# Kernel optimization log

Hardware: AMD Instinct MI355X
Metric: run time of the kernel (lower is better)

The kernel has to match this reference:

```python
import jax, jax.numpy as jnp
import numpy as np

N, D = 4096, 512
TAU, ALPHA, EPS = 0.2, 0.5, 1e-15
L2_EPS = 1e-12  # F.normalize eps


def setup_inputs() -> dict:
    key = jax.random.key(0)
    ks = jax.random.split(key, 12)
    # xavier_normal_ with gain=1.414 for [D, D] linears
    std = 1.414 * (2.0 / (D + D)) ** 0.5
    xn = lambda k: jax.random.normal(k, (D, D), jnp.float32) * std
    return {
        "z1": jax.random.normal(ks[0], (N, D), jnp.float32),
        "z2": jax.random.normal(ks[1], (N, D), jnp.float32),
        # local projector: Linear -> PReLU -> Linear
        "lw1": xn(ks[2]), "lb1": jnp.zeros((D,), jnp.float32),
        "la": jnp.full((1,), 0.25, jnp.float32),  # PReLU weight (torch default 0.25)
        "lw2": xn(ks[3]), "lb2": jnp.zeros((D,), jnp.float32),
        # global projector
        "gw1": xn(ks[4]), "gb1": jnp.zeros((D,), jnp.float32),
        "ga": jnp.full((1,), 0.25, jnp.float32),
        "gw2": xn(ks[5]), "gb2": jnp.zeros((D,), jnp.float32),
        # discriminator bilinear weight
        "W": xn(ks[6]),
        # binary positive-pair mask [N, N]
        "mask": jax.random.randint(ks[7], (N, N), 0, 2, jnp.int32),
    }


def _prelu(x, a):
    return jnp.where(x >= 0, x, a * x)


def _proj(z, w1, b1, a, w2, b2):
    # nn.Sequential(Linear, PReLU, Linear); torch Linear: z @ W.T + b
    return _prelu(z @ w1.T + b1, a[0]) @ w2.T + b2


def _l2norm(z):
    n = jnp.linalg.norm(z, axis=-1, keepdims=True)
    return z / jnp.maximum(n, L2_EPS)


def _infonce(h1, h2, m, tau):
    a = _l2norm(h1)
    b = _l2norm(h2)
    sim_intra = jnp.exp(a @ a.T / tau)  # [N, N]
    sim_inter = jnp.exp(a @ b.T / tau)  # [N, N]
    num = (sim_inter * m).sum(1)
    den = sim_intra.sum(1) + sim_inter.sum(1) - (sim_intra * m).sum(1)
    return (-jnp.log(num / den)).mean()


def reference(z1, z2, lw1, lb1, la, lw2, lb2, gw1, gb1, ga, gw2, gb2, W, mask):
    m = mask.astype(jnp.float32)
    # local (node-level) InfoNCE through the local projector
    h1 = _proj(z1, lw1, lb1, la, lw2, lb2)
    h2 = _proj(z2, lw1, lb1, la, lw2, lb2)
    local = 0.5 * (_infonce(h1, h2, m, TAU) + _infonce(h2, h1, m.T, TAU))

    # global (DGI-style) loss
    def gloss(pos_z, neg_z):
        s = pos_z.mean(0)                               # readout [D]
        h = _proj(s, gw1, gb1, ga, gw2, gb2)            # global projector [D]
        summ = W @ h                                    # [D]
        d_pos = jax.nn.sigmoid(pos_z @ summ)            # [N]
        d_neg = jax.nn.sigmoid(neg_z @ summ)            # [N]
        pos_loss = -jnp.log(d_pos + EPS).mean()
        neg_loss = -jnp.log(1.0 - d_neg + EPS).mean()
        return 0.5 * (pos_loss + neg_loss)

    glob = 0.5 * (gloss(z1, z2) + gloss(z2, z1))
    return ALPHA * local + (1.0 - ALPHA) * glob
```

## Files before the change

kernel.cpp:

```cpp
#include <hip/hip_runtime.h>
#include <math.h>

#define NN 4096
#define DD 512
#define INV_TAU 5.0f
#define EPSV 1e-15f

typedef unsigned short u16;
typedef __attribute__((ext_vector_type(8))) short short8;
typedef __attribute__((ext_vector_type(4))) float f32x4;

__device__ __forceinline__ void gld16(const void* g, void* l) {
  __builtin_amdgcn_global_load_lds(
      (const __attribute__((address_space(1))) unsigned int*)g,
      (__attribute__((address_space(3))) unsigned int*)l, 16, 0, 0);
}

__device__ __forceinline__ void bar_vm4() {
  asm volatile("s_waitcnt vmcnt(4) lgkmcnt(0)\n\ts_barrier" ::: "memory");
}
__device__ __forceinline__ void bar_vm2() {
  asm volatile("s_waitcnt vmcnt(2) lgkmcnt(0)\n\ts_barrier" ::: "memory");
}
__device__ __forceinline__ void bar_vm1() {
  asm volatile("s_waitcnt vmcnt(1) lgkmcnt(0)\n\ts_barrier" ::: "memory");
}
__device__ __forceinline__ void bar_vm0() {
  asm volatile("s_waitcnt vmcnt(0) lgkmcnt(0)\n\ts_barrier" ::: "memory");
}

__device__ __forceinline__ float bf2f(u16 u) {
  return __uint_as_float(((unsigned)u) << 16);
}
__device__ __forceinline__ u16 f2bf(float x) {
  unsigned u = __float_as_uint(x);
  u += 0x7fff + ((u >> 16) & 1);
  return (u16)(u >> 16);
}

__device__ __forceinline__ float wave_sum(float v) {
#pragma unroll
  for (int o = 32; o > 0; o >>= 1) v += __shfl_down(v, o, 64);
  return v;
}

__global__ __launch_bounds__(256) void tobf16cm(
    const float* __restrict__ a, const float* __restrict__ b,
    const float* __restrict__ c, const float* __restrict__ d2,
    u16* __restrict__ o, float* __restrict__ pc1, float* __restrict__ pc2,
    float* __restrict__ zbf) {
  const int bid = blockIdx.x, tid = threadIdx.x;
  if (bid >= 4608) {
    const int blk = bid - 4608;
    const int r0 = blk * 32;
    float a0 = 0.f, a1 = 0.f, c0 = 0.f, c1 = 0.f;
    for (int r = r0; r < r0 + 32; ++r) {
      const size_t ro = (size_t)r * DD;
      a0 += c[ro + tid];
      a1 += c[ro + 256 + tid];
      c0 += d2[ro + tid];
      c1 += d2[ro + 256 + tid];
    }
    pc1[blk * 512 + tid] = a0;
    pc1[blk * 512 + 256 + tid] = a1;
    pc2[blk * 512 + tid] = c0;
    pc2[blk * 512 + 256 + tid] = c1;
    return;
  }
  if (bid < 128) zbf[bid * 256 + tid] = 0.f;
  const int i = bid * 256 + tid;
  int j = i;
  const float* s;
  if (j < 65536) {
    s = a + (size_t)j * 4;
  } else {
    j -= 65536;
    if (j < 65536) {
      s = b + (size_t)j * 4;
    } else {
      j -= 65536;
      if (j < 524288) {
        s = c + (size_t)j * 4;
      } else {
        j -= 524288;
        s = d2 + (size_t)j * 4;
      }
    }
  }
  float4 v = *(const float4*)s;
  unsigned long long pk = (unsigned long long)f2bf(v.x) |
                          ((unsigned long long)f2bf(v.y) << 16) |
                          ((unsigned long long)f2bf(v.z) << 32) |
                          ((unsigned long long)f2bf(v.w) << 48);
  *(unsigned long long*)&o[(size_t)i * 4] = pk;
}

template <int ACT>
__global__ __launch_bounds__(512) void gemm_mfma(
    const u16* __restrict__ A, const u16* __restrict__ Bw,
    const float* __restrict__ bias, const float* __restrict__ alpha_p,
    u16* __restrict__ out) {
  __shared__ __align__(16) u16 sh[3 * 6144];
  const int tid = threadIdx.x, w = tid >> 6, lane = tid & 63;
  const int quad = lane >> 4, m16 = lane & 15;
  const int wi = w >> 1, wj = w & 1;
  const int bid = blockIdx.x;
  const int xcd = bid & 7, idx = bid >> 3;
  const int i0 = (4 * xcd + (idx & 3)) * 128;
  const int j0 = ((idx >> 2) & 7) * 64;
  const int bz = idx >> 5;
  const u16* Ab = A + (size_t)bz * ((size_t)NN * DD);
  u16* ob = out + (size_t)bz * ((size_t)NN * DD);
  const int roff =
      (m16 >> 1) * 64 + (((((m16 & 1) << 2) | quad) ^ (m16 >> 1)) * 8);
  const int st = (lane & 7) ^ (lane >> 3);
  const int srow = 2 * (lane >> 3) + (st >> 2);
  const int scol = (st & 3) * 8;
  const u16* gs = (w < 4) ? Ab : Bw;
  const int grow0 = ((w < 4) ? i0 + 2 * w * 16 : j0 + (w - 4) * 16) + srow;
  const int doff0 = (w < 4) ? 2 * w * 512 : 4096 + (w - 4) * 512;
  auto stage = [&](int bo, int k) {
    const int kn = k * 32;
    gld16(&gs[(size_t)grow0 * DD + kn + scol], sh + bo + doff0);
    if (w < 4)
      gld16(&gs[(size_t)(grow0 + 16) * DD + kn + scol], sh + bo + doff0 + 512);
  };
  stage(0, 0);
  stage(6144, 1);
  if (w < 4) bar_vm2(); else bar_vm1();
  f32x4 acc[2][2] = {};
  int ro = 0;
  for (int kc = 0; kc < 16; ++kc) {
    if (kc <= 13) {
      int so = ro + 12288;
      if (so >= 18432) so -= 18432;
      stage(so, kc + 2);
    }
    const u16* As = sh + ro;
    const u16* Bs = sh + ro + 4096;
    short8 ar[2], br[2];
#pragma unroll
    for (int s = 0; s < 2; ++s) {
      ar[s] = *(const short8*)&As[(wi * 32 + s * 16) * 32 + roff];
      br[s] = *(const short8*)&Bs[(wj * 32 + s * 16) * 32 + roff];
    }
    __builtin_amdgcn_s_setprio(1);
#pragma unroll
    for (int si = 0; si < 2; ++si)
#pragma unroll
      for (int sj = 0; sj < 2; ++sj)
        acc[si][sj] = __builtin_amdgcn_mfma_f32_16x16x32_bf16(
            ar[si], br[sj], acc[si][sj], 0, 0, 0);
    __builtin_amdgcn_s_setprio(0);
    if (kc <= 13) {
      if (w < 4) bar_vm2(); else bar_vm1();
    } else if (kc == 14) {
      bar_vm0();
    }
    ro += 6144;
    if (ro == 18432) ro = 0;
  }
  const float al = ACT ? alpha_p[0] : 0.f;
#pragma unroll
  for (int si = 0; si < 2; ++si)
#pragma unroll
    for (int sj = 0; sj < 2; ++sj) {
      const int col = j0 + wj * 32 + sj * 16 + m16;
      const float bv = bias[col];
#pragma unroll
      for (int r = 0; r < 4; ++r) {
        const int row = i0 + wi * 32 + si * 16 + quad * 4 + r;
        float x = acc[si][sj][r] + bv;
        if (ACT) x = (x >= 0.f) ? x : al * x;
        ob[(size_t)row * DD + col] = f2bf(x);
      }
    }
}

__global__ __launch_bounds__(256) void rownorm_bf16(const u16* __restrict__ h,
                                                    u16* __restrict__ o) {
  const int tid = threadIdx.x;
  const int row = blockIdx.x * 4 + (tid >> 6);
  const int lane = tid & 63;
  const size_t base = (size_t)row * DD + lane * 8;
  short8 v = *(const short8*)&h[base];
  float f[8];
  float s = 0.f;
#pragma unroll
  for (int j = 0; j < 8; ++j) {
    f[j] = bf2f((u16)v[j]);
    s += f[j] * f[j];
  }
  s = wave_sum(s);
  const float inv = 1.f / fmaxf(sqrtf(__shfl(s, 0, 64)), 1e-12f);
  short8 r;
#pragma unroll
  for (int j = 0; j < 8; ++j) r[j] = (short)f2bf(f[j] * inv);
  *(short8*)&o[base] = r;
}

__global__ __launch_bounds__(1024) void mv_chain(
    const float* __restrict__ pc1, const float* __restrict__ pc2,
    const float* __restrict__ gw1, const float* __restrict__ gb1,
    const float* __restrict__ ga, const float* __restrict__ gw2,
    const float* __restrict__ gb2, const float* __restrict__ W,
    float* __restrict__ summ1, float* __restrict__ summ2) {
  const int bz = blockIdx.x;
  const float* pc = bz ? pc2 : pc1;
  float* summ = bz ? summ2 : summ1;
  __shared__ float sv[512], tv[512], hv[512];
  const int tid = threadIdx.x;
  if (tid < 512) {
    float a = 0.f;
    for (int b = 0; b < 128; ++b) a += pc[b * 512 + tid];
    sv[tid] = a * (1.f / NN);
  }
  __syncthreads();
  const int w = tid >> 6, lane = tid & 63;
  for (int rq = 0; rq < 8; ++rq) {
    const int row = w * 32 + rq * 4;
    float a0 = 0.f, a1 = 0.f, a2 = 0.f, a3 = 0.f;
#pragma unroll
    for (int t = 0; t < 8; ++t) {
      const float x = sv[lane + 64 * t];
      a0 = fmaf(gw1[(size_t)(row + 0) * DD + lane + 64 * t], x, a0);
      a1 = fmaf(gw1[(size_t)(row + 1) * DD + lane + 64 * t], x, a1);
      a2 = fmaf(gw1[(size_t)(row + 2) * DD + lane + 64 * t], x, a2);
      a3 = fmaf(gw1[(size_t)(row + 3) * DD + lane + 64 * t], x, a3);
    }
    a0 = wave_sum(a0); a1 = wave_sum(a1); a2 = wave_sum(a2); a3 = wave_sum(a3);
    if (lane == 0) {
      const float al = ga[0];
      float v0 = a0 + gb1[row + 0], v1 = a1 + gb1[row + 1];
      float v2 = a2 + gb1[row + 2], v3 = a3 + gb1[row + 3];
      tv[row + 0] = (v0 >= 0.f) ? v0 : al * v0;
      tv[row + 1] = (v1 >= 0.f) ? v1 : al * v1;
      tv[row + 2] = (v2 >= 0.f) ? v2 : al * v2;
      tv[row + 3] = (v3 >= 0.f) ? v3 : al * v3;
    }
  }
  __syncthreads();
  for (int rq = 0; rq < 8; ++rq) {
    const int row = w * 32 + rq * 4;
    float a0 = 0.f, a1 = 0.f, a2 = 0.f, a3 = 0.f;
#pragma unroll
    for (int t = 0; t < 8; ++t) {
      const float x = tv[lane + 64 * t];
      a0 = fmaf(gw2[(size_t)(row + 0) * DD + lane + 64 * t], x, a0);
      a1 = fmaf(gw2[(size_t)(row + 1) * DD + lane + 64 * t], x, a1);
      a2 = fmaf(gw2[(size_t)(row + 2) * DD + lane + 64 * t], x, a2);
      a3 = fmaf(gw2[(size_t)(row + 3) * DD + lane + 64 * t], x, a3);
    }
    a0 = wave_sum(a0); a1 = wave_sum(a1); a2 = wave_sum(a2); a3 = wave_sum(a3);
    if (lane == 0) {
      hv[row + 0] = a0 + gb2[row + 0];
      hv[row + 1] = a1 + gb2[row + 1];
      hv[row + 2] = a2 + gb2[row + 2];
      hv[row + 3] = a3 + gb2[row + 3];
    }
  }
  __syncthreads();
  for (int rq = 0; rq < 8; ++rq) {
    const int row = w * 32 + rq * 4;
    float a0 = 0.f, a1 = 0.f, a2 = 0.f, a3 = 0.f;
#pragma unroll
    for (int t = 0; t < 8; ++t) {
      const float x = hv[lane + 64 * t];
      a0 = fmaf(W[(size_t)(row + 0) * DD + lane + 64 * t], x, a0);
      a1 = fmaf(W[(size_t)(row + 1) * DD + lane + 64 * t], x, a1);
      a2 = fmaf(W[(size_t)(row + 2) * DD + lane + 64 * t], x, a2);
      a3 = fmaf(W[(size_t)(row + 3) * DD + lane + 64 * t], x, a3);
    }
    a0 = wave_sum(a0); a1 = wave_sum(a1); a2 = wave_sum(a2); a3 = wave_sum(a3);
    if (lane == 0) {
      summ[row + 0] = a0;
      summ[row + 1] = a1;
      summ[row + 2] = a2;
      summ[row + 3] = a3;
    }
  }
}

__global__ __launch_bounds__(256) void logsigp(
    const float* __restrict__ z1, const float* __restrict__ z2,
    const float* __restrict__ sm1, const float* __restrict__ sm2,
    float* __restrict__ plsP, float* __restrict__ plsN) {
  const int ch = blockIdx.y;
  const float* z = ch ? z2 : z1;
  const float* sp = ch ? sm2 : sm1;
  const float* sn = ch ? sm1 : sm2;
  const int lane = threadIdx.x & 63;
  const int wid = threadIdx.x >> 6;
  const int row = blockIdx.x * 4 + wid;
  float dp = 0.f, dn = 0.f;
#pragma unroll
  for (int t = 0; t < 8; ++t) {
    const float zv = z[(size_t)row * DD + lane + 64 * t];
    dp = fmaf(zv, sp[lane + 64 * t], dp);
    dn = fmaf(zv, sn[lane + 64 * t], dn);
  }
  dp = wave_sum(dp);
  dn = wave_sum(dn);
  __shared__ float bp[4], bn[4];
  if (lane == 0) {
    const float sg = 1.f / (1.f + __expf(-dp));
    bp[wid] = -logf(sg + EPSV);
    const float sg2 = 1.f / (1.f + __expf(-dn));
    bn[wid] = -logf(1.f - sg2 + EPSV);
  }
  __syncthreads();
  if (threadIdx.x == 0) {
    plsP[ch * 1024 + blockIdx.x] = bp[0] + bp[1] + bp[2] + bp[3];
    plsN[ch * 1024 + blockIdx.x] = bn[0] + bn[1] + bn[2] + bn[3];
  }
}

__global__ __launch_bounds__(512) void sim_mfma(
    const u16* __restrict__ na, const u16* __restrict__ nb,
    const int* __restrict__ mask, float* __restrict__ zb) {
  extern __shared__ __align__(16) u16 shm[];
  const int tid = threadIdx.x;
  const int w = tid >> 6, lane = tid & 63;
  const int quad = lane >> 4, m16 = lane & 15;
  const int ig = w & 3, jh = w >> 2;
  const int i0 = blockIdx.y * 128, j0 = blockIdx.x * 128;
  const int roff =
      (m16 >> 1) * 64 + (((((m16 & 1) << 2) | quad) ^ (m16 >> 1)) * 8);
  const int st = (lane & 7) ^ (lane >> 3);
  const int srow = 2 * (lane >> 3) + (st >> 2);
  const int scol = (st & 3) * 8;
  const int p = w >> 1, rh = (w & 1) * 64;
  const u16* gs = (p & 1) ? nb : na;
  const int gr = ((p < 2) ? i0 : j0) + rh + srow;
  u16* dst0 = shm + p * 4096 + rh * 32;
  auto stage = [&](int bo, int k) {
    const int kn = k * 32;
#pragma unroll
    for (int rr = 0; rr < 64; rr += 16)
      gld16(&gs[(size_t)(gr + rr) * DD + kn + scol], dst0 + bo + rr * 32);
  };
  stage(0, 0);
  stage(16384, 1);
  bar_vm4();
  f32x4 a11[2][4] = {}, a12[2][4] = {}, a22[2][4] = {};
  int ro = 0;
  for (int kc = 0; kc < 16; ++kc) {
    if (kc <= 13) {
      int so = ro + 32768;
      if (so >= 49152) so -= 49152;
      stage(so, kc + 2);
    }
    const u16* Ai = shm + ro;
    const u16* Bi = shm + ro + 4096;
    const u16* Aj = shm + ro + 8192;
    const u16* Bj = shm + ro + 12288;
    short8 ai0 = *(const short8*)&Ai[(ig * 32) * 32 + roff];
    short8 ai1 = *(const short8*)&Ai[(ig * 32 + 16) * 32 + roff];
    short8 bi0 = *(const short8*)&Bi[(ig * 32) * 32 + roff];
    short8 bi1 = *(const short8*)&Bi[(ig * 32 + 16) * 32 + roff];
#pragma unroll
    for (int c = 0; c < 4; ++c) {
      short8 aj = *(const short8*)&Aj[(jh * 64 + c * 16) * 32 + roff];
      short8 bj = *(const short8*)&Bj[(jh * 64 + c * 16) * 32 + roff];
      __builtin_amdgcn_s_setprio(1);
      a11[0][c] = __builtin_amdgcn_mfma_f32_16x16x32_bf16(ai0, aj, a11[0][c], 0, 0, 0);
      a11[1][c] = __builtin_amdgcn_mfma_f32_16x16x32_bf16(ai1, aj, a11[1][c], 0, 0, 0);
      a12[0][c] = __builtin_amdgcn_mfma_f32_16x16x32_bf16(ai0, bj, a12[0][c], 0, 0, 0);
      a12[1][c] = __builtin_amdgcn_mfma_f32_16x16x32_bf16(ai1, bj, a12[1][c], 0, 0, 0);
      a22[0][c] = __builtin_amdgcn_mfma_f32_16x16x32_bf16(bi0, bj, a22[0][c], 0, 0, 0);
      a22[1][c] = __builtin_amdgcn_mfma_f32_16x16x32_bf16(bi1, bj, a22[1][c], 0, 0, 0);
      __builtin_amdgcn_s_setprio(0);
    }
    if (kc <= 13) bar_vm4();
    else if (kc == 14) bar_vm0();
    ro += 16384;
    if (ro == 49152) ro = 0;
  }
  float* rred = (float*)(shm + 16384);
  float* cred = rred + 512;
  rred[tid] = 0.f;
  rred[tid + 512] = 0.f;
  __syncthreads();
  float rs11[2][4] = {}, rm11[2][4] = {}, rs12[2][4] = {}, rm12[2][4] = {};
  float cs12[4] = {}, cm12[4] = {}, cs22[4] = {}, cm22[4] = {};
#pragma unroll
  for (int t = 0; t < 2; ++t)
#pragma unroll
    for (int c = 0; c < 4; ++c) {
      const int gj = j0 + jh * 64 + c * 16 + m16;
#pragma unroll
      for (int r = 0; r < 4; ++r) {
        const int gi = i0 + ig * 32 + t * 16 + quad * 4 + r;
        const float mv = (float)mask[(size_t)gi * NN + gj];
        const float e11 = __expf(a11[t][c][r] * INV_TAU);
        const float e12 = __expf(a12[t][c][r] * INV_TAU);
        const float e22 = __expf(a22[t][c][r] * INV_TAU);
        rs11[t][r] += e11;
        rm11[t][r] += e11 * mv;
        rs12[t][r] += e12;
        rm12[t][r] += e12 * mv;
        cs12[c] += e12;
        cm12[c] += e12 * mv;
        cs22[c] += e22;
        cm22[c] += e22 * mv;
      }
    }
#pragma unroll
  for (int t = 0; t < 2; ++t)
#pragma unroll
    for (int r = 0; r < 4; ++r) {
      float v0 = rs11[t][r], v1 = rm11[t][r], v2 = rs12[t][r], v3 = rm12[t][r];
#pragma unroll
      for (int o = 1; o < 16; o <<= 1) {
        v0 += __shfl_xor(v0, o, 64);
        v1 += __shfl_xor(v1, o, 64);
        v2 += __shfl_xor(v2, o, 64);
        v3 += __shfl_xor(v3, o, 64);
      }
      if (m16 == 0) {
        const int il = ig * 32 + t * 16 + quad * 4 + r;
        atomicAdd(&rred[0 * 128 + il], v0);
        atomicAdd(&rred[1 * 128 + il], v1);
        atomicAdd(&rred[2 * 128 + il], v2);
        atomicAdd(&rred[3 * 128 + il], v3);
      }
    }
#pragma unroll
  for (int c = 0; c < 4; ++c) {
    float v0 = cs12[c], v1 = cm12[c], v2 = cs22[c], v3 = cm22[c];
    v0 += __shfl_xor(v0, 16, 64); v0 += __shfl_xor(v0, 32, 64);
    v1 += __shfl_xor(v1, 16, 64); v1 += __shfl_xor(v1, 32, 64);
    v2 += __shfl_xor(v2, 16, 64); v2 += __shfl_xor(v2, 32, 64);
    v3 += __shfl_xor(v3, 16, 64); v3 += __shfl_xor(v3, 32, 64);
    if (lane < 16) {
      const int jl = jh * 64 + c * 16 + lane;
      atomicAdd(&cred[0 * 128 + jl], v0);
      atomicAdd(&cred[1 * 128 + jl], v1);
      atomicAdd(&cred[2 * 128 + jl], v2);
      atomicAdd(&cred[3 * 128 + jl], v3);
    }
  }
  __syncthreads();
  if (tid < 128) {
#pragma unroll
    for (int q = 0; q < 4; ++q)
      atomicAdd(&zb[q * NN + i0 + tid], rred[q * 128 + tid]);
  } else if (tid < 256) {
    const int jl = tid - 128;
#pragma unroll
    for (int q = 0; q < 4; ++q)
      atomicAdd(&zb[(4 + q) * NN + j0 + jl], cred[q * 128 + jl]);
  }
}

__global__ __launch_bounds__(512) void fin(const float* __restrict__ zb,
                                           const float* __restrict__ plsP,
                                           const float* __restrict__ plsN,
                                           float* __restrict__ out) {
  const int tid = threadIdx.x;
  const int lane = tid & 63, w = tid >> 6;
  float S1 = 0.f, S2 = 0.f;
#pragma unroll
  for (int k = 0; k < 8; ++k) {
    const int i = tid + k * 512;
    const float r11 = zb[i], r11m = zb[NN + i];
    const float r12 = zb[2 * NN + i], r12m = zb[3 * NN + i];
    const float c12 = zb[4 * NN + i], c12m = zb[5 * NN + i];
    const float c22 = zb[6 * NN + i], c22m = zb[7 * NN + i];
    S1 += -logf(r12m / (r11 + r12 - r11m));
    S2 += -logf(c12m / (c22 + c12 - c22m));
  }
  float G = plsP[tid] + plsP[tid + 512] + plsP[tid + 1024] + plsP[tid + 1536] +
            plsN[tid] + plsN[tid + 512] + plsN[tid + 1024] + plsN[tid + 1536];
  S1 = wave_sum(S1);
  S2 = wave_sum(S2);
  G = wave_sum(G);
  __shared__ float fr[3][8];
  if (lane == 0) { fr[0][w] = S1; fr[1][w] = S2; fr[2][w] = G; }
  __syncthreads();
  if (tid == 0) {
    float s1t = 0.f, s2t = 0.f, gt = 0.f;
    for (int q = 0; q < 8; ++q) {
      s1t += fr[0][q];
      s2t += fr[1][q];
      gt += fr[2][q];
    }
    const float local = 0.5f * (s1t + s2t) * (1.f / NN);
    const float glob = 0.25f * gt * (1.f / NN);
    out[0] = 0.5f * local + 0.5f * glob;
  }
}

extern "C" void kernel_launch(void* const* d_in, const int* in_sizes, int n_in,
                              void* d_out, int out_size, void* d_ws,
                              size_t ws_size, hipStream_t stream) {
  const float* z1 = (const float*)d_in[0];
  const float* z2 = (const float*)d_in[1];
  const float* lw1 = (const float*)d_in[2];
  const float* lb1 = (const float*)d_in[3];
  const float* la = (const float*)d_in[4];
  const float* lw2 = (const float*)d_in[5];
  const float* lb2 = (const float*)d_in[6];
  const float* gw1 = (const float*)d_in[7];
  const float* gb1 = (const float*)d_in[8];
  const float* ga = (const float*)d_in[9];
  const float* gw2 = (const float*)d_in[10];
  const float* gb2 = (const float*)d_in[11];
  const float* W = (const float*)d_in[12];
  const int* mask = (const int*)d_in[13];
  float* out = (float*)d_out;

  static bool attr_set = false;
  if (!attr_set) {
    (void)hipFuncSetAttribute(reinterpret_cast<const void*>(sim_mfma),
                              hipFuncAttributeMaxDynamicSharedMemorySize,
                              98304);
    attr_set = true;
  }

  const size_t ND = (size_t)NN * DD;
  u16* W1b = (u16*)d_ws;
  u16* W2b = W1b + 512 * 512;
  u16* Ab = W1b + 2 * 512 * 512;
  u16* Bb = Ab + 2 * ND;
  float* zbf = (float*)(Bb + 2 * ND);
  float* pc1 = zbf + 8 * NN;
  float* pc2 = pc1 + 128 * 512;
  float* summ1 = pc2 + 128 * 512;
  float* summ2 = summ1 + 512;
  float* plsP = summ2 + 512;
  float* plsN = plsP + 2048;

  dim3 blk(256);
  tobf16cm<<<4736, blk, 0, stream>>>(lw1, lw2, z1, z2, W1b, pc1, pc2, zbf);
  gemm_mfma<1><<<512, dim3(512), 0, stream>>>(Ab, W1b, lb1, la, Bb);
  gemm_mfma<0><<<512, dim3(512), 0, stream>>>(Bb, W2b, lb2, la, Ab);
  rownorm_bf16<<<2048, blk, 0, stream>>>(Ab, Bb);
  mv_chain<<<2, dim3(1024), 0, stream>>>(pc1, pc2, gw1, gb1, ga, gw2, gb2, W,
                                         summ1, summ2);
  logsigp<<<dim3(1024, 2), blk, 0, stream>>>(z1, z2, summ1, summ2, plsP, plsN);
  sim_mfma<<<dim3(32, 32), dim3(512), 98304, stream>>>(Bb, Bb + ND, mask, zbf);
  fin<<<1, dim3(512), 0, stream>>>(zbf, plsP, plsN, out);
}
```

Measured before the change: 302.6 us.

## Fold global-branch matvec chain and logsig into existing GEMM/rownorm/sim kernels

Removes the two-block serial mv_chain kernel and the separate logsigp kernel. Each matvec stage now runs as extra blocks inside the local GEMM, rownorm, and similarity launches, and the logsig reduction becomes two extra block rows in sim_mfma. This cuts two launches and replaces a poorly parallel 2-block kernel with work spread across many blocks. In exchange, the fused kernels become heterogeneous and the extra blocks may delay the main tiles; the GEMM XCD mapping is also shifted by 64 blocks.

```diff
diff --git a/kernel.cpp b/kernel.cpp
--- a/kernel.cpp
+++ b/kernel.cpp
@@ -96,16 +96,53 @@
 }
 
 template <int ACT>
-__global__ __launch_bounds__(512) void gemm_mfma(
+__global__ __launch_bounds__(512) void gemm_mv(
     const u16* __restrict__ A, const u16* __restrict__ Bw,
     const float* __restrict__ bias, const float* __restrict__ alpha_p,
-    u16* __restrict__ out) {
+    u16* __restrict__ out, const float* __restrict__ Mw,
+    const float* __restrict__ mx1, const float* __restrict__ mx2,
+    const float* __restrict__ mbias, const float* __restrict__ mal,
+    float* __restrict__ my1, float* __restrict__ my2) {
   __shared__ __align__(16) u16 sh[3 * 6144];
+  __shared__ float svb[512];
   const int tid = threadIdx.x, w = tid >> 6, lane = tid & 63;
+  if (blockIdx.x < 64) {
+    const int mb = blockIdx.x;
+    const int bz = mb >> 5, bx = mb & 31;
+    const float* xin = bz ? mx2 : mx1;
+    float* y = bz ? my2 : my1;
+    if (ACT) {
+      float a = 0.f;
+      for (int b = 0; b < 128; ++b) a += xin[b * 512 + tid];
+      svb[tid] = a * (1.f / NN);
+    } else {
+      svb[tid] = xin[tid];
+    }
+    __syncthreads();
+#pragma unroll
+    for (int rr = 0; rr < 2; ++rr) {
+      const int row = bx * 16 + w * 2 + rr;
+      float acc = 0.f;
+#pragma unroll
+      for (int q = 0; q < 8; ++q)
+        acc = fmaf(Mw[(size_t)row * DD + lane + 64 * q], svb[lane + 64 * q],
+                   acc);
+      acc = wave_sum(acc);
+      if (lane == 0) {
+        acc += mbias[row];
+        if (ACT) {
+          const float al = mal[0];
+          acc = (acc >= 0.f) ? acc : al * acc;
+        }
+        y[row] = acc;
+      }
+    }
+    return;
+  }
   const int quad = lane >> 4, m16 = lane & 15;
   const int wi = w >> 1, wj = w & 1;
-  const int bid = blockIdx.x;
-  const int xcd = bid & 7, idx = bid >> 3;
+  const int bid2 = blockIdx.x - 64;
+  const int xcd = bid2 & 7, idx = bid2 >> 3;
   const int i0 = (4 * xcd + (idx & 3)) * 128;
   const int j0 = ((idx >> 2) & 7) * 64;
   const int bz = idx >> 5;
@@ -177,11 +214,27 @@
     }
 }
 
-__global__ __launch_bounds__(256) void rownorm_bf16(const u16* __restrict__ h,
-                                                    u16* __restrict__ o) {
-  const int tid = threadIdx.x;
-  const int row = blockIdx.x * 4 + (tid >> 6);
-  const int lane = tid & 63;
+__global__ __launch_bounds__(256) void rownorm_mv(
+    const u16* __restrict__ h, u16* __restrict__ o,
+    const float* __restrict__ W, const float* __restrict__ hx1,
+    const float* __restrict__ hx2, float* __restrict__ sm1,
+    float* __restrict__ sm2) {
+  const int bid = blockIdx.x, tid = threadIdx.x;
+  const int lane = tid & 63, w = tid >> 6;
+  if (bid < 256) {
+    const int bz = bid >> 7, bx = bid & 127;
+    const float* x = bz ? hx2 : hx1;
+    float* y = bz ? sm2 : sm1;
+    const int row = bx * 4 + w;
+    float acc = 0.f;
+#pragma unroll
+    for (int q = 0; q < 8; ++q)
+      acc = fmaf(W[(size_t)row * DD + lane + 64 * q], x[lane + 64 * q], acc);
+    acc = wave_sum(acc);
+    if (lane == 0) y[row] = acc;
+    return;
+  }
+  const int row = (bid - 256) * 4 + w;
   const size_t base = (size_t)row * DD + lane * 8;
   short8 v = *(const short8*)&h[base];
   float f[8];
@@ -199,131 +252,52 @@
   *(short8*)&o[base] = r;
 }
 
-__global__ __launch_bounds__(1024) void mv_chain(
-    const float* __restrict__ pc1, const float* __restrict__ pc2,
-    const float* __restrict__ gw1, const float* __restrict__ gb1,
-    const float* __restrict__ ga, const float* __restrict__ gw2,
-    const float* __restrict__ gb2, const float* __restrict__ W,
-    float* __restrict__ summ1, float* __restrict__ summ2) {
-  const int bz = blockIdx.x;
-  const float* pc = bz ? pc2 : pc1;
-  float* summ = bz ? summ2 : summ1;
-  __shared__ float sv[512], tv[512], hv[512];
-  const int tid = threadIdx.x;
-  if (tid < 512) {
-    float a = 0.f;
-    for (int b = 0; b < 128; ++b) a += pc[b * 512 + tid];
-    sv[tid] = a * (1.f / NN);
-  }
-  __syncthreads();
-  const int w = tid >> 6, lane = tid & 63;
-  for (int rq = 0; rq < 8; ++rq) {
-    const int row = w * 32 + rq * 4;
-    float a0 = 0.f, a1 = 0.f, a2 = 0.f, a3 = 0.f;
-#pragma unroll
-    for (int t = 0; t < 8; ++t) {
-      const float x = sv[lane + 64 * t];
-      a0 = fmaf(gw1[(size_t)(row + 0) * DD + lane + 64 * t], x, a0);
-      a1 = fmaf(gw1[(size_t)(row + 1) * DD + lane + 64 * t], x, a1);
-      a2 = fmaf(gw1[(size_t)(row + 2) * DD + lane + 64 * t], x, a2);
-      a3 = fmaf(gw1[(size_t)(row + 3) * DD + lane + 64 * t], x, a3);
-    }
-    a0 = wave_sum(a0); a1 = wave_sum(a1); a2 = wave_sum(a2); a3 = wave_sum(a3);
-    if (lane == 0) {
-      const float al = ga[0];
-      float v0 = a0 + gb1[row + 0], v1 = a1 + gb1[row + 1];
-      float v2 = a2 + gb1[row + 2], v3 = a3 + gb1[row + 3];
-      tv[row + 0] = (v0 >= 0.f) ? v0 : al * v0;
-      tv[row + 1] = (v1 >= 0.f) ? v1 : al * v1;
-      tv[row + 2] = (v2 >= 0.f) ? v2 : al * v2;
-      tv[row + 3] = (v3 >= 0.f) ? v3 : al * v3;
-    }
-  }
-  __syncthreads();
-  for (int rq = 0; rq < 8; ++rq) {
-    const int row = w * 32 + rq * 4;
-    float a0 = 0.f, a1 = 0.f, a2 = 0.f, a3 = 0.f;
-#pragma unroll
-    for (int t = 0; t < 8; ++t) {
-      const float x = tv[lane + 64 * t];
-      a0 = fmaf(gw2[(size_t)(row + 0) * DD + lane + 64 * t], x, a0);
-      a1 = fmaf(gw2[(size_t)(row + 1) * DD + lane + 64 * t], x, a1);
-      a2 = fmaf(gw2[(size_t)(row + 2) * DD + lane + 64 * t], x, a2);
-      a3 = fmaf(gw2[(size_t)(row + 3) * DD + lane + 64 * t], x, a3);
-    }
-    a0 = wave_sum(a0); a1 = wave_sum(a1); a2 = wave_sum(a2); a3 = wave_sum(a3);
-    if (lane == 0) {
-      hv[row + 0] = a0 + gb2[row + 0];
-      hv[row + 1] = a1 + gb2[row + 1];
-      hv[row + 2] = a2 + gb2[row + 2];
-      hv[row + 3] = a3 + gb2[row + 3];
-    }
-  }
-  __syncthreads();
-  for (int rq = 0; rq < 8; ++rq) {
-    const int row = w * 32 + rq * 4;
-    float a0 = 0.f, a1 = 0.f, a2 = 0.f, a3 = 0.f;
-#pragma unroll
-    for (int t = 0; t < 8; ++t) {
-      const float x = hv[lane + 64 * t];
-      a0 = fmaf(W[(size_t)(row + 0) * DD + lane + 64 * t], x, a0);
-      a1 = fmaf(W[(size_t)(row + 1) * DD + lane + 64 * t], x, a1);
-      a2 = fmaf(W[(size_t)(row + 2) * DD + lane + 64 * t], x, a2);
-      a3 = fmaf(W[(size_t)(row + 3) * DD + lane + 64 * t], x, a3);
-    }
-    a0 = wave_sum(a0); a1 = wave_sum(a1); a2 = wave_sum(a2); a3 = wave_sum(a3);
-    if (lane == 0) {
-      summ[row + 0] = a0;
-      summ[row + 1] = a1;
-      summ[row + 2] = a2;
-      summ[row + 3] = a3;
-    }
-  }
-}
-
-__global__ __launch_bounds__(256) void logsigp(
-    const float* __restrict__ z1, const float* __restrict__ z2,
+__global__ __launch_bounds__(512) void sim_mfma(
+    const u16* __restrict__ na, const u16* __restrict__ nb,
+    const int* __restrict__ mask, float* __restrict__ zb,
+    const float* __restrict__ z1g, const float* __restrict__ z2g,
     const float* __restrict__ sm1, const float* __restrict__ sm2,
     float* __restrict__ plsP, float* __restrict__ plsN) {
-  const int ch = blockIdx.y;
-  const float* z = ch ? z2 : z1;
-  const float* sp = ch ? sm2 : sm1;
-  const float* sn = ch ? sm1 : sm2;
-  const int lane = threadIdx.x & 63;
-  const int wid = threadIdx.x >> 6;
-  const int row = blockIdx.x * 4 + wid;
-  float dp = 0.f, dn = 0.f;
-#pragma unroll
-  for (int t = 0; t < 8; ++t) {
-    const float zv = z[(size_t)row * DD + lane + 64 * t];
-    dp = fmaf(zv, sp[lane + 64 * t], dp);
-    dn = fmaf(zv, sn[lane + 64 * t], dn);
-  }
-  dp = wave_sum(dp);
-  dn = wave_sum(dn);
-  __shared__ float bp[4], bn[4];
-  if (lane == 0) {
-    const float sg = 1.f / (1.f + __expf(-dp));
-    bp[wid] = -logf(sg + EPSV);
-    const float sg2 = 1.f / (1.f + __expf(-dn));
-    bn[wid] = -logf(1.f - sg2 + EPSV);
-  }
-  __syncthreads();
-  if (threadIdx.x == 0) {
-    plsP[ch * 1024 + blockIdx.x] = bp[0] + bp[1] + bp[2] + bp[3];
-    plsN[ch * 1024 + blockIdx.x] = bn[0] + bn[1] + bn[2] + bn[3];
-  }
-}
-
-__global__ __launch_bounds__(512) void sim_mfma(
-    const u16* __restrict__ na, const u16* __restrict__ nb,
-    const int* __restrict__ mask, float* __restrict__ zb) {
   extern __shared__ __align__(16) u16 shm[];
   const int tid = threadIdx.x;
   const int w = tid >> 6, lane = tid & 63;
+  if (blockIdx.y < 2) {
+    const int lx = blockIdx.y * 32 + blockIdx.x;
+    const int bz = lx >> 5, bx5 = lx & 31;
+    const float* z = bz ? z2g : z1g;
+    const float* sp = bz ? sm2 : sm1;
+    const float* sn = bz ? sm1 : sm2;
+    float lp = 0.f, ln_ = 0.f;
+    for (int k = 0; k < 16; ++k) {
+      const int row = bx5 * 128 + w * 16 + k;
+      float dp = 0.f, dn = 0.f;
+#pragma unroll
+      for (int t = 0; t < 8; ++t) {
+        const float zv = z[(size_t)row * DD + lane + 64 * t];
+        dp = fmaf(zv, sp[lane + 64 * t], dp);
+        dn = fmaf(zv, sn[lane + 64 * t], dn);
+      }
+      dp = wave_sum(dp);
+      dn = wave_sum(dn);
+      if (lane == 0) {
+        lp += -logf(1.f / (1.f + __expf(-dp)) + EPSV);
+        ln_ += -logf(1.f - 1.f / (1.f + __expf(-dn)) + EPSV);
+      }
+    }
+    float* red = (float*)shm;
+    if (lane == 0) { red[w] = lp; red[8 + w] = ln_; }
+    __syncthreads();
+    if (tid == 0) {
+      float sP = 0.f, sN = 0.f;
+      for (int q = 0; q < 8; ++q) { sP += red[q]; sN += red[8 + q]; }
+      plsP[lx] = sP;
+      plsN[lx] = sN;
+    }
+    return;
+  }
   const int quad = lane >> 4, m16 = lane & 15;
   const int ig = w & 3, jh = w >> 2;
-  const int i0 = blockIdx.y * 128, j0 = blockIdx.x * 128;
+  const int i0 = (blockIdx.y - 2) * 128, j0 = blockIdx.x * 128;
   const int roff =
       (m16 >> 1) * 64 + (((((m16 & 1) << 2) | quad) ^ (m16 >> 1)) * 8);
   const int st = (lane & 7) ^ (lane >> 3);
@@ -470,8 +444,7 @@
     S1 += -logf(r12m / (r11 + r12 - r11m));
     S2 += -logf(c12m / (c22 + c12 - c22m));
   }
-  float G = plsP[tid] + plsP[tid + 512] + plsP[tid + 1024] + plsP[tid + 1536] +
-            plsN[tid] + plsN[tid + 512] + plsN[tid + 1024] + plsN[tid + 1536];
+  float G = (tid < 64) ? (plsP[tid] + plsN[tid]) : 0.f;
   S1 = wave_sum(S1);
   S2 = wave_sum(S2);
   G = wave_sum(G);
@@ -526,19 +499,24 @@
   float* zbf = (float*)(Bb + 2 * ND);
   float* pc1 = zbf + 8 * NN;
   float* pc2 = pc1 + 128 * 512;
-  float* summ1 = pc2 + 128 * 512;
+  float* t1 = pc2 + 128 * 512;
+  float* t2 = t1 + 512;
+  float* hg1 = t2 + 512;
+  float* hg2 = hg1 + 512;
+  float* summ1 = hg2 + 512;
   float* summ2 = summ1 + 512;
   float* plsP = summ2 + 512;
-  float* plsN = plsP + 2048;
-
-  dim3 blk(256);
-  tobf16cm<<<4736, blk, 0, stream>>>(lw1, lw2, z1, z2, W1b, pc1, pc2, zbf);
-  gemm_mfma<1><<<512, dim3(512), 0, stream>>>(Ab, W1b, lb1, la, Bb);
-  gemm_mfma<0><<<512, dim3(512), 0, stream>>>(Bb, W2b, lb2, la, Ab);
-  rownorm_bf16<<<2048, blk, 0, stream>>>(Ab, Bb);
-  mv_chain<<<2, dim3(1024), 0, stream>>>(pc1, pc2, gw1, gb1, ga, gw2, gb2, W,
-                                         summ1, summ2);
-  logsigp<<<dim3(1024, 2), blk, 0, stream>>>(z1, z2, summ1, summ2, plsP, plsN);
-  sim_mfma<<<dim3(32, 32), dim3(512), 98304, stream>>>(Bb, Bb + ND, mask, zbf);
+  float* plsN = plsP + 64;
+
+  tobf16cm<<<4736, dim3(256), 0, stream>>>(lw1, lw2, z1, z2, W1b, pc1, pc2,
+                                           zbf);
+  gemm_mv<1><<<576, dim3(512), 0, stream>>>(Ab, W1b, lb1, la, Bb, gw1, pc1,
+                                            pc2, gb1, ga, t1, t2);
+  gemm_mv<0><<<576, dim3(512), 0, stream>>>(Bb, W2b, lb2, la, Ab, gw2, t1, t2,
+                                            gb2, nullptr, hg1, hg2);
+  rownorm_mv<<<2304, dim3(256), 0, stream>>>(Ab, Bb, W, hg1, hg2, summ1,
+                                             summ2);
+  sim_mfma<<<dim3(32, 34), dim3(512), 98304, stream>>>(
+      Bb, Bb + ND, mask, zbf, z1, z2, summ1, summ2, plsP, plsN);
   fin<<<1, dim3(512), 0, stream>>>(zbf, plsP, plsN, out);
 }
```

New measurement: 257.2 us. 1.18x faster.
